# Kernel optimization log

Measured on AMD Instinct MI355X. Metric: run time of the kernel, lower is better.

## Reference

```python
import jax, jax.numpy as jnp
import numpy as np

N = 100000   # num nodes
E = 1600000  # num edges (avg degree 16)
C = 64       # channels
L = 3        # num_layers


def setup_inputs() -> dict:
    key = jax.random.key(0)
    k1, k2, k3 = jax.random.split(key, 3)
    x = jax.random.normal(k1, (N, C), dtype=jnp.float32)
    # per-layer GCNConv weights: channels -> 2*channels (glorot-ish scale)
    Ws = jax.random.normal(k2, (L, C, 2 * C), dtype=jnp.float32) / np.sqrt(C)
    bs = jnp.zeros((L, 2 * C), dtype=jnp.float32)
    edge_index = jax.random.randint(k3, (2, E), 0, N, dtype=jnp.int64)
    return {"x": x, "Ws": Ws, "bs": bs, "edge_index": edge_index}


def _gcn_layer(x, W, b, src, dst, dinv):
    # GCNConv with self-loops and symmetric normalization D^-1/2 A_hat D^-1/2
    h = x @ W                                   # [N, 2C]
    coef = dinv[src] * dinv[dst]                # [E] edge norm
    agg = jax.ops.segment_sum(h[src] * coef[:, None], dst,
                              num_segments=x.shape[0])  # scatter-add to targets
    # self-loop contribution has norm dinv[i]^2
    return agg + h * (dinv * dinv)[:, None] + b


def reference(x, Ws, bs, edge_index):
    src, dst = edge_index[0], edge_index[1]
    n = x.shape[0]
    # degree after adding self-loops (count incoming edges at target + 1)
    deg = jnp.zeros((n,), x.dtype).at[dst].add(jnp.asarray(1.0, x.dtype)) + 1.0
    dinv = jax.lax.rsqrt(deg)
    for l in range(Ws.shape[0]):  # small fixed layer count
        residual = x
        h = _gcn_layer(x, Ws[l], bs[l], src, dst, dinv)
        a, g = jnp.split(h, 2, axis=-1)
        x = a * jax.nn.sigmoid(g) + residual   # GLU + residual
    return x
```

## Files before the change

kernel.cpp:

```cpp
#include <hip/hip_runtime.h>
#include <math.h>

#define NNODES 100000
#define NEDGES 1600000
#define CH 64
#define CH2 128
#define NLAYERS 3
#define NBLK 98
#define NPB 512
#define NBKT 196
#define BKT_CAP 10240
#define CHUNK 8192
#define KPT 32

typedef unsigned int uint;
typedef unsigned short ushort;

__device__ __forceinline__ ushort f2bf(float f) {
    uint u = __float_as_uint(f);
    u = (u + 0x7fffu + ((u >> 16) & 1u)) >> 16;
    return (ushort)u;
}
__device__ __forceinline__ float bflo(uint p) { return __uint_as_float(p << 16); }
__device__ __forceinline__ float bfhi(uint p) { return __uint_as_float(p & 0xffff0000u); }


__global__ void binit_kernel(int* __restrict__ bcur) {
    int b = blockIdx.x * 256 + threadIdx.x;
    if (b < NBKT) bcur[b] = b * BKT_CAP;
}

__global__ __launch_bounds__(256) void bfill2_kernel(const int* __restrict__ src,
                                                     const int* __restrict__ dst,
                                                     int* __restrict__ bcur,
                                                     int2* __restrict__ epair) {
    __shared__ int hcnt[NBKT];
    __shared__ int hbase[NBKT];
    int t = threadIdx.x;
    int e0 = blockIdx.x * CHUNK;

    for (int b = t; b < NBKT; b += 256) hcnt[b] = 0;
    __syncthreads();

#pragma unroll
    for (int i = 0; i < KPT; ++i) {
        int e = e0 + i * 256 + t;
        if (e < NEDGES) atomicAdd(&hcnt[dst[e] >> 9], 1);
    }
    __syncthreads();

    for (int b = t; b < NBKT; b += 256) {
        int c = hcnt[b];
        hbase[b] = c ? atomicAdd(&bcur[b], c) : 0;
        hcnt[b] = 0;
    }
    __syncthreads();

#pragma unroll
    for (int i = 0; i < KPT; ++i) {
        int e = e0 + i * 256 + t;
        if (e < NEDGES) {
            int s = src[e];
            int d = dst[e];
            int bkt = d >> 9;
            int r = atomicAdd(&hcnt[bkt], 1);
            epair[hbase[bkt] + r] = make_int2(s, d);
        }
    }
}

__global__ __launch_bounds__(256) void bcount_kernel(const int* __restrict__ bcur,
                                                     const int2* __restrict__ epair,
                                                     int* __restrict__ cnt) {
    __shared__ int lcnt[NPB];
    int b = blockIdx.x;
    int n0 = b * NPB;
    int n1 = n0 + NPB; if (n1 > NNODES) n1 = NNODES;
    int t = threadIdx.x;
    for (int i = t; i < NPB; i += 256) lcnt[i] = 0;
    __syncthreads();
    int seg0 = b * BKT_CAP;
    int seg1 = bcur[b];
    for (int i = seg0 + t; i < seg1; i += 256) {
        int d = epair[i].y;
        atomicAdd(&lcnt[d - n0], 1);
    }
    __syncthreads();
    for (int i = t; i < n1 - n0; i += 256) cnt[n0 + i] = lcnt[i];
}

__global__ void dinv_kernel(const int* __restrict__ cnt, float* __restrict__ dinv, int n) {
    int t = blockIdx.x * blockDim.x + threadIdx.x;
    if (t < n) dinv[t] = rsqrtf((float)cnt[t] + 1.0f);
}


__global__ __launch_bounds__(256) void bsum_kernel(const int* __restrict__ cnt,
                                                   int* __restrict__ bsum) {
    int t = threadIdx.x;
    int base = blockIdx.x * 1024 + t * 4;
    int s = 0;
#pragma unroll
    for (int i = 0; i < 4; ++i) { int k = base + i; if (k < NNODES) s += cnt[k]; }
    __shared__ int ls[256];
    ls[t] = s; __syncthreads();
    for (int off = 128; off > 0; off >>= 1) {
        if (t < off) ls[t] += ls[t + off];
        __syncthreads();
    }
    if (t == 0) bsum[blockIdx.x] = ls[0];
}

__global__ __launch_bounds__(128) void bscan_kernel(const int* __restrict__ bsum,
                                                    int* __restrict__ boff,
                                                    int* __restrict__ rowptr) {
    __shared__ int s[128];
    int t = threadIdx.x;
    int v = (t < NBLK) ? bsum[t] : 0;
    s[t] = v; __syncthreads();
    for (int off = 1; off < 128; off <<= 1) {
        int u = (t >= off) ? s[t - off] : 0;
        __syncthreads();
        s[t] += u;
        __syncthreads();
    }
    if (t < NBLK) boff[t] = s[t] - v;
    if (t == 0) rowptr[NNODES] = NEDGES;
}

__global__ __launch_bounds__(256) void scanb_kernel(const int* __restrict__ cnt,
                                                    const int* __restrict__ boff,
                                                    int* __restrict__ rowptr) {
    int t = threadIdx.x;
    int base = blockIdx.x * 1024 + t * 4;
    int v[4]; int tsum = 0;
#pragma unroll
    for (int i = 0; i < 4; ++i) { int k = base + i; v[i] = (k < NNODES) ? cnt[k] : 0; tsum += v[i]; }
    __shared__ int ls[256];
    ls[t] = tsum; __syncthreads();
    for (int off = 1; off < 256; off <<= 1) {
        int u = (t >= off) ? ls[t - off] : 0;
        __syncthreads();
        ls[t] += u;
        __syncthreads();
    }
    int run = boff[blockIdx.x] + ls[t] - tsum;
#pragma unroll
    for (int i = 0; i < 4; ++i) {
        int k = base + i;
        if (k < NNODES) { rowptr[k] = run; run += v[i]; }
    }
}

__global__ __launch_bounds__(256) void bsort_kernel(const int* __restrict__ rowptr,
                                                    const int* __restrict__ bcur,
                                                    const int2* __restrict__ epair,
                                                    int* __restrict__ esrc) {
    __shared__ int cur[NPB];
    int b = blockIdx.x;
    int n0 = b * NPB;
    if (n0 >= NNODES) return;
    int n1 = n0 + NPB; if (n1 > NNODES) n1 = NNODES;
    int t = threadIdx.x;
    for (int i = t; i < n1 - n0; i += 256) cur[i] = rowptr[n0 + i];
    __syncthreads();
    int seg0 = b * BKT_CAP;
    int seg1 = bcur[b];
    for (int i = seg0 + t; i < seg1; i += 256) {
        int2 p = epair[i];
        int pos = atomicAdd(&cur[p.y - n0], 1);
        esrc[pos] = p.x;
    }
}


__global__ __launch_bounds__(256) void y0_kernel(const float* __restrict__ x,
                                                 const float* __restrict__ dinv,
                                                 ushort* __restrict__ y) {
    int t = blockIdx.x * 256 + threadIdx.x;
    if (t >= NNODES * CH) return;
    int node = t >> 6;
    y[t] = f2bf(dinv[node] * x[t]);
}


__global__ __launch_bounds__(256) void agg8_kernel(const int* __restrict__ rowptr,
                                                   const int* __restrict__ esrc,
                                                   const ushort* __restrict__ y,
                                                   const float* __restrict__ dinv,
                                                   float* __restrict__ z) {
    int w = (blockIdx.x * 256 + threadIdx.x) >> 6;
    int lane = threadIdx.x & 63;
    if (w >= NNODES) return;
    int g = lane >> 3;
    int q = lane & 7;

    int start = rowptr[w];
    int end   = rowptr[w + 1];
    float acc[8];
#pragma unroll
    for (int i = 0; i < 8; ++i) acc[i] = 0.0f;

    for (int base = start; base < end; base += 64) {
        int m = end - base; if (m > 64) m = 64;
        int e = (lane < m) ? esrc[base + lane] : 0;
        int m8 = m & ~7;
        int j = 0;
#pragma unroll 2
        for (; j < m8; j += 8) {
            int s = __shfl(e, j + g, 64);
            uint4 v = *(const uint4*)(y + (size_t)s * CH + q * 8);
            acc[0] += bflo(v.x); acc[1] += bfhi(v.x);
            acc[2] += bflo(v.y); acc[3] += bfhi(v.y);
            acc[4] += bflo(v.z); acc[5] += bfhi(v.z);
            acc[6] += bflo(v.w); acc[7] += bfhi(v.w);
        }
        if (m8 < m) {
            int s = __shfl(e, m8 + g, 64);
            if (m8 + g < m) {
                uint4 v = *(const uint4*)(y + (size_t)s * CH + q * 8);
                acc[0] += bflo(v.x); acc[1] += bfhi(v.x);
                acc[2] += bflo(v.y); acc[3] += bfhi(v.y);
                acc[4] += bflo(v.z); acc[5] += bfhi(v.z);
                acc[6] += bflo(v.w); acc[7] += bfhi(v.w);
            }
        }
    }

#pragma unroll
    for (int off = 8; off < 64; off <<= 1) {
#pragma unroll
        for (int i = 0; i < 8; ++i)
            acc[i] += __shfl_xor(acc[i], off, 64);
    }

    if (lane < 8) {
        uint4 sv = *(const uint4*)(y + (size_t)w * CH + lane * 8);
        float dv = dinv[w];
        float4 o0, o1;
        o0.x = dv * (acc[0] + bflo(sv.x));
        o0.y = dv * (acc[1] + bfhi(sv.x));
        o0.z = dv * (acc[2] + bflo(sv.y));
        o0.w = dv * (acc[3] + bfhi(sv.y));
        o1.x = dv * (acc[4] + bflo(sv.z));
        o1.y = dv * (acc[5] + bfhi(sv.z));
        o1.z = dv * (acc[6] + bflo(sv.w));
        o1.w = dv * (acc[7] + bfhi(sv.w));
        *(float4*)(z + (size_t)w * CH + lane * 8)     = o0;
        *(float4*)(z + (size_t)w * CH + lane * 8 + 4) = o1;
    }
}


__global__ __launch_bounds__(256) void gemm_glu_kernel(const float* __restrict__ z,
                                                       const float* __restrict__ W,
                                                       const float* __restrict__ b,
                                                       const float* __restrict__ xold,
                                                       const float* __restrict__ dinv,
                                                       float* __restrict__ xnew,
                                                       ushort* __restrict__ ynext,
                                                       int write_y) {
    __shared__ float Wl[CH * CH2];
    __shared__ float Zl[16 * CH];
    int t = threadIdx.x;

    const float4* W4 = (const float4*)W;
    float4* Wl4 = (float4*)Wl;
#pragma unroll
    for (int i = 0; i < 8; ++i) Wl4[t + 256 * i] = W4[t + 256 * i];

    int row0 = blockIdx.x * 16;
    ((float4*)Zl)[t] = ((const float4*)(z + (size_t)row0 * CH))[t];
    __syncthreads();

    int c  = t & 63;
    int rg = t >> 6;
    float accA[4] = {0.f, 0.f, 0.f, 0.f};
    float accG[4] = {0.f, 0.f, 0.f, 0.f};

#pragma unroll 4
    for (int k = 0; k < CH; ++k) {
        float wa = Wl[k * CH2 + c];
        float wg = Wl[k * CH2 + 64 + c];
#pragma unroll
        for (int i = 0; i < 4; ++i) {
            float zv = Zl[(rg * 4 + i) * CH + k];
            accA[i] += zv * wa;
            accG[i] += zv * wg;
        }
    }

    float ba = b[c], bg = b[64 + c];
#pragma unroll
    for (int i = 0; i < 4; ++i) {
        int row = row0 + rg * 4 + i;
        size_t idx = (size_t)row * CH + c;
        float a = accA[i] + ba;
        float gv = accG[i] + bg;
        float sg = 1.0f / (1.0f + expf(-gv));
        float xv = a * sg + xold[idx];
        xnew[idx] = xv;
        if (write_y)
            ynext[idx] = f2bf(dinv[row] * xv);
    }
}


extern "C" void kernel_launch(void* const* d_in, const int* in_sizes, int n_in,
                              void* d_out, int out_size, void* d_ws, size_t ws_size,
                              hipStream_t stream) {
    const float* x_in = (const float*)d_in[0];
    const float* Ws   = (const float*)d_in[1];
    const float* bs   = (const float*)d_in[2];
    const int*   ei   = (const int*)d_in[3];
    const int* src = ei;
    const int* dst = ei + NEDGES;

    char* wsb = (char*)d_ws;
    int*    cnt    = (int*)wsb;
    float*  dinv   = (float*)(wsb + 512 * 1024);
    int*    rowptr = (int*)(wsb + 1024 * 1024);
    int*    bsum   = (int*)(wsb + 1536 * 1024);
    int*    boff   = bsum + 128;
    int*    bcur   = (int*)(wsb + 1792 * 1024);
    int*    esrc   = (int*)(wsb + 2 * 1024 * 1024);
    int2*   epair  = (int2*)(wsb + 9 * 1024 * 1024);
    ushort* y      = (ushort*)(wsb + 26 * 1024 * 1024);
    float*  z      = (float*)(wsb + 39 * 1024 * 1024);
    float*  xbuf   = (float*)(wsb + 65 * 1024 * 1024);

    binit_kernel<<<1, 256, 0, stream>>>(bcur);
    bfill2_kernel<<<(NEDGES + CHUNK - 1) / CHUNK, 256, 0, stream>>>(src, dst, bcur, epair);
    bcount_kernel<<<NBKT, 256, 0, stream>>>(bcur, epair, cnt);
    dinv_kernel<<<(NNODES + 255) / 256, 256, 0, stream>>>(cnt, dinv, NNODES);
    bsum_kernel<<<NBLK, 256, 0, stream>>>(cnt, bsum);
    bscan_kernel<<<1, 128, 0, stream>>>(bsum, boff, rowptr);
    scanb_kernel<<<NBLK, 256, 0, stream>>>(cnt, boff, rowptr);
    bsort_kernel<<<NBKT, 256, 0, stream>>>(rowptr, bcur, epair, esrc);
    y0_kernel<<<(NNODES * CH + 255) / 256, 256, 0, stream>>>(x_in, dinv, y);

    const float* xl = x_in;
    for (int l = 0; l < NLAYERS; ++l) {
        const float* W = Ws + (size_t)l * CH * CH2;
        const float* b = bs + (size_t)l * CH2;
        float* xout = (l == NLAYERS - 1) ? (float*)d_out : xbuf;

        agg8_kernel<<<(NNODES * 64 + 255) / 256, 256, 0, stream>>>(rowptr, esrc, y, dinv, z);
        gemm_glu_kernel<<<NNODES / 16, 256, 0, stream>>>(z, W, b, xl, dinv, xout, y,
                                                         (l < NLAYERS - 1) ? 1 : 0);

        xl = xout;
    }
}
```

Before: 396.8 us.

## Use bf16 MFMA for the GEMM+GLU stage with prepacked weight fragments

Replaces the scalar fp32 shared-memory GEMM with a wave-level bf16 MFMA 16x16x32 kernel. Weights are converted once into per-lane fragment layout by a new wconv kernel. The aggregation output z is stored as bf16 instead of fp32, which halves its write and read traffic. The trade is lower precision in the GEMM input and weights, plus one extra small launch.

```diff
diff --git a/kernel.cpp b/kernel.cpp
--- a/kernel.cpp
+++ b/kernel.cpp
@@ -15,6 +15,8 @@
 
 typedef unsigned int uint;
 typedef unsigned short ushort;
+typedef __attribute__((ext_vector_type(8))) short bf16x8;
+typedef __attribute__((ext_vector_type(4))) float f32x4;
 
 __device__ __forceinline__ ushort f2bf(float f) {
     uint u = __float_as_uint(f);
@@ -23,6 +25,11 @@
 }
 __device__ __forceinline__ float bflo(uint p) { return __uint_as_float(p << 16); }
 __device__ __forceinline__ float bfhi(uint p) { return __uint_as_float(p & 0xffff0000u); }
+
+union U8 { uint4 u; bf16x8 v; ushort s[8]; };
+__device__ __forceinline__ bf16x8 ld8(const ushort* p) {
+    U8 t; t.u = *(const uint4*)p; return t.v;
+}
 
 
 __global__ void binit_kernel(int* __restrict__ bcur) {
@@ -184,11 +191,29 @@
 }
 
 
+__global__ void wconv_kernel(const float* __restrict__ Ws, ushort* __restrict__ Wfrag) {
+    int t = blockIdx.x * 256 + threadIdx.x;
+    if (t >= NLAYERS * 8 * 2 * 64) return;
+    int lane = t & 63;
+    int kh = (t >> 6) & 1;
+    int n = (t >> 7) & 7;
+    int l = t >> 10;
+    ushort o[8];
+#pragma unroll
+    for (int j = 0; j < 8; ++j) {
+        int k = kh * 32 + (lane >> 4) * 8 + j;
+        int col = n * 16 + (lane & 15);
+        o[j] = f2bf(Ws[(size_t)l * CH * CH2 + (size_t)k * CH2 + col]);
+    }
+    *(uint4*)(Wfrag + (size_t)t * 8) = *(uint4*)o;
+}
+
+
 __global__ __launch_bounds__(256) void agg8_kernel(const int* __restrict__ rowptr,
                                                    const int* __restrict__ esrc,
                                                    const ushort* __restrict__ y,
                                                    const float* __restrict__ dinv,
-                                                   float* __restrict__ z) {
+                                                   ushort* __restrict__ z) {
     int w = (blockIdx.x * 256 + threadIdx.x) >> 6;
     int lane = threadIdx.x & 63;
     if (w >= NNODES) return;
@@ -237,71 +262,69 @@
     if (lane < 8) {
         uint4 sv = *(const uint4*)(y + (size_t)w * CH + lane * 8);
         float dv = dinv[w];
-        float4 o0, o1;
-        o0.x = dv * (acc[0] + bflo(sv.x));
-        o0.y = dv * (acc[1] + bfhi(sv.x));
-        o0.z = dv * (acc[2] + bflo(sv.y));
-        o0.w = dv * (acc[3] + bfhi(sv.y));
-        o1.x = dv * (acc[4] + bflo(sv.z));
-        o1.y = dv * (acc[5] + bfhi(sv.z));
-        o1.z = dv * (acc[6] + bflo(sv.w));
-        o1.w = dv * (acc[7] + bfhi(sv.w));
-        *(float4*)(z + (size_t)w * CH + lane * 8)     = o0;
-        *(float4*)(z + (size_t)w * CH + lane * 8 + 4) = o1;
-    }
-}
-
-
-__global__ __launch_bounds__(256) void gemm_glu_kernel(const float* __restrict__ z,
-                                                       const float* __restrict__ W,
-                                                       const float* __restrict__ b,
-                                                       const float* __restrict__ xold,
-                                                       const float* __restrict__ dinv,
-                                                       float* __restrict__ xnew,
-                                                       ushort* __restrict__ ynext,
-                                                       int write_y) {
-    __shared__ float Wl[CH * CH2];
-    __shared__ float Zl[16 * CH];
-    int t = threadIdx.x;
-
-    const float4* W4 = (const float4*)W;
-    float4* Wl4 = (float4*)Wl;
-#pragma unroll
-    for (int i = 0; i < 8; ++i) Wl4[t + 256 * i] = W4[t + 256 * i];
-
-    int row0 = blockIdx.x * 16;
-    ((float4*)Zl)[t] = ((const float4*)(z + (size_t)row0 * CH))[t];
-    __syncthreads();
-
-    int c  = t & 63;
-    int rg = t >> 6;
-    float accA[4] = {0.f, 0.f, 0.f, 0.f};
-    float accG[4] = {0.f, 0.f, 0.f, 0.f};
-
-#pragma unroll 4
-    for (int k = 0; k < CH; ++k) {
-        float wa = Wl[k * CH2 + c];
-        float wg = Wl[k * CH2 + 64 + c];
-#pragma unroll
-        for (int i = 0; i < 4; ++i) {
-            float zv = Zl[(rg * 4 + i) * CH + k];
-            accA[i] += zv * wa;
-            accG[i] += zv * wg;
+        U8 o;
+        o.s[0] = f2bf(dv * (acc[0] + bflo(sv.x)));
+        o.s[1] = f2bf(dv * (acc[1] + bfhi(sv.x)));
+        o.s[2] = f2bf(dv * (acc[2] + bflo(sv.y)));
+        o.s[3] = f2bf(dv * (acc[3] + bfhi(sv.y)));
+        o.s[4] = f2bf(dv * (acc[4] + bflo(sv.z)));
+        o.s[5] = f2bf(dv * (acc[5] + bfhi(sv.z)));
+        o.s[6] = f2bf(dv * (acc[6] + bflo(sv.w)));
+        o.s[7] = f2bf(dv * (acc[7] + bfhi(sv.w)));
+        *(uint4*)(z + (size_t)w * CH + lane * 8) = o.u;
+    }
+}
+
+
+__global__ __launch_bounds__(256) void gemm_glu_mfma_kernel(const ushort* __restrict__ z,
+                                                            const ushort* __restrict__ Wfrag,
+                                                            const float* __restrict__ b,
+                                                            const float* __restrict__ xold,
+                                                            const float* __restrict__ dinv,
+                                                            float* __restrict__ xnew,
+                                                            ushort* __restrict__ ynext,
+                                                            int write_y) {
+    int wid  = threadIdx.x >> 6;
+    int lane = threadIdx.x & 63;
+    int row0 = blockIdx.x * 64 + wid * 16;
+    if (row0 >= NNODES) return;
+    int rl = lane & 15;
+    int h  = lane >> 4;
+
+    const ushort* zp = z + (size_t)(row0 + rl) * CH + h * 8;
+    bf16x8 a0 = ld8(zp);
+    bf16x8 a1 = ld8(zp + 32);
+
+    f32x4 acc[8];
+#pragma unroll
+    for (int n = 0; n < 8; ++n) {
+        bf16x8 b0 = ld8(Wfrag + ((size_t)(n * 2 + 0) * 64 + lane) * 8);
+        bf16x8 b1 = ld8(Wfrag + ((size_t)(n * 2 + 1) * 64 + lane) * 8);
+        f32x4 c = {0.f, 0.f, 0.f, 0.f};
+        c = __builtin_amdgcn_mfma_f32_16x16x32_bf16(a0, b0, c, 0, 0, 0);
+        c = __builtin_amdgcn_mfma_f32_16x16x32_bf16(a1, b1, c, 0, 0, 0);
+        acc[n] = c;
+    }
+
+    float ba[4], bg[4];
+#pragma unroll
+    for (int n = 0; n < 4; ++n) { ba[n] = b[n * 16 + rl]; bg[n] = b[64 + n * 16 + rl]; }
+
+#pragma unroll
+    for (int reg = 0; reg < 4; ++reg) {
+        int row = row0 + h * 4 + reg;
+        float dv = dinv[row];
+#pragma unroll
+        for (int n = 0; n < 4; ++n) {
+            int c = n * 16 + rl;
+            size_t idx = (size_t)row * CH + c;
+            float a  = acc[n][reg] + ba[n];
+            float gv = acc[n + 4][reg] + bg[n];
+            float sg = 1.0f / (1.0f + expf(-gv));
+            float xv = a * sg + xold[idx];
+            xnew[idx] = xv;
+            if (write_y) ynext[idx] = f2bf(dv * xv);
         }
-    }
-
-    float ba = b[c], bg = b[64 + c];
-#pragma unroll
-    for (int i = 0; i < 4; ++i) {
-        int row = row0 + rg * 4 + i;
-        size_t idx = (size_t)row * CH + c;
-        float a = accA[i] + ba;
-        float gv = accG[i] + bg;
-        float sg = 1.0f / (1.0f + expf(-gv));
-        float xv = a * sg + xold[idx];
-        xnew[idx] = xv;
-        if (write_y)
-            ynext[idx] = f2bf(dinv[row] * xv);
     }
 }
 
@@ -323,11 +346,12 @@
     int*    bsum   = (int*)(wsb + 1536 * 1024);
     int*    boff   = bsum + 128;
     int*    bcur   = (int*)(wsb + 1792 * 1024);
+    ushort* Wfrag  = (ushort*)(wsb + 1856 * 1024);
     int*    esrc   = (int*)(wsb + 2 * 1024 * 1024);
     int2*   epair  = (int2*)(wsb + 9 * 1024 * 1024);
     ushort* y      = (ushort*)(wsb + 26 * 1024 * 1024);
-    float*  z      = (float*)(wsb + 39 * 1024 * 1024);
-    float*  xbuf   = (float*)(wsb + 65 * 1024 * 1024);
+    ushort* z      = (ushort*)(wsb + 39 * 1024 * 1024);
+    float*  xbuf   = (float*)(wsb + 52 * 1024 * 1024);
 
     binit_kernel<<<1, 256, 0, stream>>>(bcur);
     bfill2_kernel<<<(NEDGES + CHUNK - 1) / CHUNK, 256, 0, stream>>>(src, dst, bcur, epair);
@@ -337,17 +361,18 @@
     bscan_kernel<<<1, 128, 0, stream>>>(bsum, boff, rowptr);
     scanb_kernel<<<NBLK, 256, 0, stream>>>(cnt, boff, rowptr);
     bsort_kernel<<<NBKT, 256, 0, stream>>>(rowptr, bcur, epair, esrc);
+    wconv_kernel<<<(NLAYERS * 1024 + 255) / 256, 256, 0, stream>>>(Ws, Wfrag);
     y0_kernel<<<(NNODES * CH + 255) / 256, 256, 0, stream>>>(x_in, dinv, y);
 
     const float* xl = x_in;
     for (int l = 0; l < NLAYERS; ++l) {
-        const float* W = Ws + (size_t)l * CH * CH2;
-        const float* b = bs + (size_t)l * CH2;
+        const ushort* Wf = Wfrag + (size_t)l * 1024 * 8;
+        const float*  b  = bs + (size_t)l * CH2;
         float* xout = (l == NLAYERS - 1) ? (float*)d_out : xbuf;
 
         agg8_kernel<<<(NNODES * 64 + 255) / 256, 256, 0, stream>>>(rowptr, esrc, y, dinv, z);
-        gemm_glu_kernel<<<NNODES / 16, 256, 0, stream>>>(z, W, b, xl, dinv, xout, y,
-                                                         (l < NLAYERS - 1) ? 1 : 0);
+        gemm_glu_mfma_kernel<<<(NNODES + 63) / 64, 256, 0, stream>>>(z, Wf, b, xl, dinv, xout, y,
+                                                                     (l < NLAYERS - 1) ? 1 : 0);
 
         xl = xout;
     }
```

Result: faster. 329.9 us (-16.9%).
